# Kernel tuning notes

Measured on AMD Instinct MI355X. Metric: run time of the kernel, lower is better.

The kernel has to match this reference:

```python
import jax, jax.numpy as jnp
import numpy as np

GROUPS = 32
N_HEADS = 8
EPS = 1e-5


def setup_inputs() -> dict:
    key = jax.random.key(0)
    ks = jax.random.split(key, 4)
    B, C, H, W = 8, 512, 32, 32
    x = jax.random.normal(ks[0], (B, C, H, W), dtype=jnp.float32)
    norm_scale = jnp.ones((C,), jnp.float32)
    norm_bias = jnp.zeros((C,), jnp.float32)
    qkv_w = jax.random.normal(ks[1], (3 * C, C), jnp.float32) * (C ** -0.5)
    qkv_b = jnp.zeros((3 * C,), jnp.float32)
    proj_w = jax.random.normal(ks[2], (C, C), jnp.float32) * (C ** -0.5)
    proj_b = jnp.zeros((C,), jnp.float32)
    return {"x": x, "norm_scale": norm_scale, "norm_bias": norm_bias,
            "qkv_w": qkv_w, "qkv_b": qkv_b, "proj_w": proj_w, "proj_b": proj_b}


def reference(x, norm_scale, norm_bias, qkv_w, qkv_b, proj_w, proj_b):
    B, C, H, W = x.shape
    T = H * W
    xf = x.reshape(B, C, T)

    # GroupNorm32 (32 groups, computed in float32, affine)
    xg = xf.astype(jnp.float32).reshape(B, GROUPS, C // GROUPS, T)
    mean = xg.mean(axis=(2, 3), keepdims=True)
    var = xg.var(axis=(2, 3), keepdims=True)
    xn = ((xg - mean) * jax.lax.rsqrt(var + EPS)).reshape(B, C, T)
    xn = (xn * norm_scale[:, None] + norm_bias[:, None]).astype(x.dtype)

    # qkv: 1x1 conv1d == pointwise matmul -> [B, 3C, T]
    qkv = jnp.einsum('oc,bct->bot', qkv_w, xn) + qkv_b[:, None]

    # QKVAttentionLegacy: reshape to [B*H, 3*ch, T], split
    ch = C // N_HEADS
    qkv_h = qkv.reshape(B * N_HEADS, 3 * ch, T)
    q, k, v = qkv_h[:, :ch], qkv_h[:, ch:2 * ch], qkv_h[:, 2 * ch:]
    scale = ch ** -0.25
    weight = jnp.einsum('bct,bcs->bts', q * scale, k * scale)  # [B*H, T, T]
    weight = jax.nn.softmax(weight.astype(jnp.float32), axis=-1).astype(qkv.dtype)
    a = jnp.einsum('bts,bcs->bct', weight, v).reshape(B, C, T)

    # proj_out (1x1 conv) + residual
    h = jnp.einsum('oc,bct->bot', proj_w, a) + proj_b[:, None]
    return (xf + h).reshape(B, C, H, W)
```

## Files before the change

kernel.cpp:

```cpp
#include <hip/hip_runtime.h>
#include <hip/hip_bf16.h>
#include <stdint.h>

typedef unsigned short u16;
typedef unsigned int u32;
typedef __bf16 bf16x8 __attribute__((ext_vector_type(8)));
typedef float f32x4 __attribute__((ext_vector_type(4)));


static __device__ __forceinline__ u16 f2bf(float f) {
  union { __hip_bfloat16 h; u16 u; } c;
  c.h = __float2bfloat16(f);
  return c.u;
}

static __device__ __forceinline__ void gload_lds16(const void* g, void* l) {
  __builtin_amdgcn_global_load_lds(
      (__attribute__((address_space(1))) u32*)(uintptr_t)g,
      (__attribute__((address_space(3))) u32*)l, 16, 0, 0);
}

__global__ __launch_bounds__(256) void wcvt(const float* __restrict__ wq,
                                            const float* __restrict__ wp,
                                            u16* __restrict__ wqb,
                                            u16* __restrict__ wpb) {
  int idx = (blockIdx.x * 256 + threadIdx.x) * 4;
  const float* s;
  u16* d;
  if (idx < 786432) { s = wq + idx; d = wqb + idx; }
  else { int k = idx - 786432; s = wp + k; d = wpb + k; }
  float4 v = *(const float4*)s;
  uint2 o;
  o.x = (u32)f2bf(v.x) | ((u32)f2bf(v.y) << 16);
  o.y = (u32)f2bf(v.z) | ((u32)f2bf(v.w) << 16);
  *(uint2*)d = o;
}

__global__ __launch_bounds__(256) void gn_stats(const float* __restrict__ x,
                                                float* __restrict__ st) {
  int bg = blockIdx.x;
  const float* p = x + (size_t)bg * 16384;
  float s1 = 0.f, s2 = 0.f;
  for (int i = threadIdx.x * 4; i < 16384; i += 1024) {
    float4 v = *(const float4*)(p + i);
    s1 += v.x + v.y + v.z + v.w;
    s2 += v.x * v.x + v.y * v.y + v.z * v.z + v.w * v.w;
  }
#pragma unroll
  for (int off = 1; off < 64; off <<= 1) {
    s1 += __shfl_xor(s1, off);
    s2 += __shfl_xor(s2, off);
  }
  __shared__ float r1[4], r2[4];
  int w = threadIdx.x >> 6, l = threadIdx.x & 63;
  if (l == 0) { r1[w] = s1; r2[w] = s2; }
  __syncthreads();
  if (threadIdx.x == 0) {
    float t1 = r1[0] + r1[1] + r1[2] + r1[3];
    float t2 = r2[0] + r2[1] + r2[2] + r2[3];
    float mean = t1 * (1.f / 16384.f);
    float var = t2 * (1.f / 16384.f) - mean * mean;
    st[bg * 2] = mean;
    st[bg * 2 + 1] = rsqrtf(var + 1e-5f);
  }
}

__global__ __launch_bounds__(256) void gn_apply(const float* __restrict__ x,
                                                const float* __restrict__ st,
                                                const float* __restrict__ ns,
                                                const float* __restrict__ nbi,
                                                u16* __restrict__ xnt) {
  __shared__ u16 tile[32 * 520];
  int b = blockIdx.x >> 5;
  int t0 = (blockIdx.x & 31) << 5;
  int tid = threadIdx.x;
  int tl = tid & 31, cg = tid >> 5;
#pragma unroll 4
  for (int cc = 0; cc < 64; ++cc) {
    int c = cc * 8 + cg;
    float mean = st[(b * 32 + (c >> 4)) * 2];
    float rstd = st[(b * 32 + (c >> 4)) * 2 + 1];
    float v = x[(size_t)b * 524288 + (size_t)c * 1024 + t0 + tl];
    float vn = (v - mean) * rstd * ns[c] + nbi[c];
    tile[tl * 520 + c] = f2bf(vn);
  }
  __syncthreads();
#pragma unroll
  for (int i = 0; i < 8; ++i) {
    int chunk = i * 256 + tid;
    int tl2 = chunk >> 6;
    int c0 = (chunk & 63) * 8;
    uint4 d = *(const uint4*)(tile + tl2 * 520 + c0);
    *(uint4*)(xnt + (size_t)b * 524288 + (size_t)(t0 + tl2) * 512 + c0) = d;
  }
}

static __device__ __forceinline__ void gemm_core(const u16* Abase, const u16* Bbase,
                                                 f32x4 acc[4][4], u16* As, u16* Bs,
                                                 int w, int l, int wm, int wn) {
  const int r8 = l >> 3, ch = l & 7;
  const int fr = l & 15, fq = l >> 4;
#pragma unroll 1
  for (int kt = 0; kt < 8; ++kt) {
    __syncthreads();
#pragma unroll
    for (int i = 0; i < 4; ++i) {
      int gi = (w << 2) + i;
      int row = (gi << 3) + r8;
      int xoff = ((ch ^ (row & 7)) << 4);
      gload_lds16((const char*)Abase + (size_t)row * 1024 + (kt << 7) + xoff,
                  (char*)As + (gi << 10));
      gload_lds16((const char*)Bbase + (size_t)row * 1024 + (kt << 7) + xoff,
                  (char*)Bs + (gi << 10));
    }
    __syncthreads();
#pragma unroll
    for (int kf = 0; kf < 2; ++kf) {
      bf16x8 af[4], bfv[4];
#pragma unroll
      for (int i = 0; i < 4; ++i) {
        int rowA = wm * 64 + i * 16 + fr;
        af[i] = *(const bf16x8*)(As + rowA * 64 + ((((kf << 2) + fq) ^ (rowA & 7)) << 3));
        int rowB = wn * 64 + i * 16 + fr;
        bfv[i] = *(const bf16x8*)(Bs + rowB * 64 + ((((kf << 2) + fq) ^ (rowB & 7)) << 3));
      }
#pragma unroll
      for (int i = 0; i < 4; ++i)
#pragma unroll
        for (int j = 0; j < 4; ++j)
          acc[i][j] = __builtin_amdgcn_mfma_f32_16x16x32_bf16(af[i], bfv[j], acc[i][j], 0, 0, 0);
    }
  }
}

__global__ __launch_bounds__(256) void gemm_qkv(const u16* __restrict__ Wq,
                                                const u16* __restrict__ Xnt,
                                                const float* __restrict__ bq,
                                                u16* __restrict__ qT,
                                                u16* __restrict__ kT,
                                                u16* __restrict__ vv) {
  __shared__ u16 SMEM[18432];
  int bid0 = blockIdx.x;
  int bid = (bid0 & 7) * 96 + (bid0 >> 3);
  int mb = bid % 12, nb = (bid / 12) % 8, b = bid / 96;
  int tid = threadIdx.x, w = tid >> 6, l = tid & 63;
  int wm = tid >> 7, wn = (tid >> 6) & 1;
  int fr = l & 15, fq = l >> 4;
  f32x4 acc[4][4];
#pragma unroll
  for (int i = 0; i < 4; ++i)
#pragma unroll
    for (int j = 0; j < 4; ++j) acc[i][j] = (f32x4){0.f, 0.f, 0.f, 0.f};

  gemm_core(Wq + (size_t)mb * 65536, Xnt + (size_t)b * 524288 + (size_t)nb * 65536,
            acc, SMEM, SMEM + 8192, w, l, wm, wn);

  __syncthreads();

  int seg2 = mb * 2 + wm;
  int h = seg2 / 3, typ = seg2 % 3;
  size_t hb = (size_t)(b * 8 + h) * 65536;
  u16* SUB = SMEM + wm * 9216;

  if (typ < 2) {
    float qksc = (typ == 0) ? 0.51011687f : 0.35355339f;
#pragma unroll
    for (int i = 0; i < 4; ++i) {
      int oi = i * 16 + fq * 4;
      float4 bb = *(const float4*)(bq + mb * 128 + wm * 64 + oi);
#pragma unroll
      for (int j = 0; j < 4; ++j) {
        int tl = wn * 64 + j * 16 + fr;
        f32x4 v = acc[i][j];
        u32 lo = (u32)f2bf((v[0] + bb.x) * qksc) | ((u32)f2bf((v[1] + bb.y) * qksc) << 16);
        u32 hi = (u32)f2bf((v[2] + bb.z) * qksc) | ((u32)f2bf((v[3] + bb.w) * qksc) << 16);
        *(u32*)(SUB + tl * 72 + oi) = lo;
        *(u32*)(SUB + tl * 72 + oi + 2) = hi;
      }
    }
  } else {
#pragma unroll
    for (int i = 0; i < 4; ++i) {
      int oi = i * 16 + fq * 4;
      float4 bb = *(const float4*)(bq + mb * 128 + wm * 64 + oi);
      float bbv[4] = {bb.x, bb.y, bb.z, bb.w};
#pragma unroll
      for (int j = 0; j < 4; ++j) {
        int tl = wn * 64 + j * 16 + fr;
        f32x4 v = acc[i][j];
#pragma unroll
        for (int r = 0; r < 4; ++r)
          SUB[(oi + r) * 136 + tl] = f2bf(v[r] + bbv[r]);
      }
    }
  }
  __syncthreads();

  int lt = tid & 127;
  if (typ < 2) {
    u16* dstb = (typ == 0 ? qT : kT) + hb;
#pragma unroll
    for (int it = 0; it < 8; ++it) {
      int slot = it * 128 + lt;
      int t = slot >> 3, chk = slot & 7;
      uint4 val = *(const uint4*)(SUB + t * 72 + chk * 8);
      *(uint4*)(dstb + (size_t)(nb * 128 + t) * 64 + chk * 8) = val;
    }
  } else {
#pragma unroll
    for (int it = 0; it < 8; ++it) {
      int slot = it * 128 + lt;
      int c = slot >> 4, chk = slot & 15;
      uint4 val = *(const uint4*)(SUB + c * 136 + chk * 8);
      *(uint4*)(vv + hb + (size_t)c * 1024 + nb * 128 + chk * 8) = val;
    }
  }
}

__global__ __launch_bounds__(512) void attn(const u16* __restrict__ qT,
                                            const u16* __restrict__ kT,
                                            const u16* __restrict__ vv,
                                            u16* __restrict__ aT) {
  __shared__ u16 Ks[128 * 64];
  __shared__ u16 Vs[64 * 128];
  __shared__ u16 Ps[8 * 16 * 72];
  int bid = blockIdx.x;
  int bh = (bid & 7) * 8 + (bid >> 6);
  int tq = (bid >> 3) & 7;
  int tid = threadIdx.x, w = tid >> 6, l = tid & 63;
  int fr = l & 15, fq = l >> 4;
  int r8 = l >> 3, ch = l & 7;
  size_t hb = (size_t)bh * 65536;

  bf16x8 aq[2];
  {
    const u16* qp = qT + hb + (size_t)(tq * 128 + w * 16 + fr) * 64 + fq * 8;
    aq[0] = *(const bf16x8*)(qp);
    aq[1] = *(const bf16x8*)(qp + 32);
  }

  union { u32 u[4]; bf16x8 v; } onesu;
#pragma unroll
  for (int i = 0; i < 4; ++i) onesu.u[i] = 0x3F803F80u;
  const bf16x8 vone = onesu.v;

  f32x4 acc_o[4];
  f32x4 acc_s = (f32x4){0.f, 0.f, 0.f, 0.f};
#pragma unroll
  for (int nb = 0; nb < 4; ++nb) acc_o[nb] = (f32x4){0.f, 0.f, 0.f, 0.f};

  u16* pw = Ps + w * (16 * 72);

#pragma unroll 1
  for (int st = 0; st < 8; ++st) {
    __syncthreads();
#pragma unroll
    for (int j = 0; j < 2; ++j) {
      int gi = w * 2 + j;
      int row = gi * 8 + r8;
      int xoff = ((ch ^ (row & 7)) << 4);
      gload_lds16((const char*)(kT + hb) + (size_t)(st * 128 + row) * 128 + xoff,
                  (char*)Ks + (gi << 10));
      int c = gi * 4 + (l >> 4);
      int half = (l >> 3) & 1;
      int ch8 = l & 7;
      int sxoff = half * 128 + ((ch8 ^ (c & 7)) << 4);
      gload_lds16((const char*)(vv + hb) + (size_t)c * 2048 + st * 256 + sxoff,
                  (char*)Vs + (gi << 10));
    }
    __syncthreads();

#pragma unroll
    for (int sh = 0; sh < 2; ++sh) {
      f32x4 sa[4];
#pragma unroll
      for (int nb = 0; nb < 4; ++nb) sa[nb] = (f32x4){0.f, 0.f, 0.f, 0.f};
      __builtin_amdgcn_s_setprio(1);
#pragma unroll
      for (int nb = 0; nb < 4; ++nb) {
        int krow = sh * 64 + nb * 16 + fr;
#pragma unroll
        for (int kf = 0; kf < 2; ++kf) {
          bf16x8 bk = *(const bf16x8*)(Ks + krow * 64 + ((((kf << 2) + fq) ^ (krow & 7)) << 3));
          sa[nb] = __builtin_amdgcn_mfma_f32_16x16x32_bf16(aq[kf], bk, sa[nb], 0, 0, 0);
        }
      }
      __builtin_amdgcn_s_setprio(0);

#pragma unroll
      for (int nb = 0; nb < 4; ++nb)
#pragma unroll
        for (int r = 0; r < 4; ++r)
          pw[(fq * 4 + r) * 72 + nb * 16 + fr] = f2bf(exp2f(sa[nb][r]));

      bf16x8 ap[2];
#pragma unroll
      for (int kf = 0; kf < 2; ++kf)
        ap[kf] = *(const bf16x8*)(pw + fr * 72 + kf * 32 + fq * 8);

      __builtin_amdgcn_s_setprio(1);
#pragma unroll
      for (int nb = 0; nb < 4; ++nb) {
        int vrow = nb * 16 + fr;
#pragma unroll
        for (int kf = 0; kf < 2; ++kf) {
          bf16x8 bv = *(const bf16x8*)(Vs + vrow * 128 + sh * 64 +
                                       ((((kf << 2) + fq) ^ (vrow & 7)) << 3));
          acc_o[nb] = __builtin_amdgcn_mfma_f32_16x16x32_bf16(ap[kf], bv, acc_o[nb], 0, 0, 0);
        }
      }
#pragma unroll
      for (int kf = 0; kf < 2; ++kf)
        acc_s = __builtin_amdgcn_mfma_f32_16x16x32_bf16(ap[kf], vone, acc_s, 0, 0, 0);
      __builtin_amdgcn_s_setprio(0);
    }
  }

  int b = bh >> 3, h = bh & 7;
  f32x4 invl;
#pragma unroll
  for (int r = 0; r < 4; ++r) invl[r] = 1.f / acc_s[r];
#pragma unroll
  for (int nb = 0; nb < 4; ++nb) {
    f32x4 ov = acc_o[nb] * invl;
#pragma unroll
    for (int r = 0; r < 4; ++r) {
      int t = tq * 128 + w * 16 + fq * 4 + r;
      aT[(size_t)b * 524288 + (size_t)t * 512 + h * 64 + nb * 16 + fr] = f2bf(ov[r]);
    }
  }
}

__global__ __launch_bounds__(256) void gemm_proj(const u16* __restrict__ Wp,
                                                 const u16* __restrict__ aT,
                                                 const float* __restrict__ bp,
                                                 const float* __restrict__ x,
                                                 float* __restrict__ out) {
  __shared__ u16 As[128 * 64];
  __shared__ u16 Bs[128 * 64];
  int bid0 = blockIdx.x;
  int bid = (bid0 & 7) * 32 + (bid0 >> 3);
  int mb = bid & 3, nb = (bid >> 2) & 7, b = bid >> 5;
  int tid = threadIdx.x, w = tid >> 6, l = tid & 63;
  int wm = w >> 1, wn = w & 1;
  f32x4 acc[4][4];
#pragma unroll
  for (int i = 0; i < 4; ++i)
#pragma unroll
    for (int j = 0; j < 4; ++j) acc[i][j] = (f32x4){0.f, 0.f, 0.f, 0.f};

  gemm_core(Wp + (size_t)mb * 65536, aT + (size_t)b * 524288 + (size_t)nb * 65536,
            acc, As, Bs, w, l, wm, wn);

  int fr = l & 15, fq = l >> 4;
#pragma unroll
  for (int i = 0; i < 4; ++i) {
    int o0 = mb * 128 + wm * 64 + i * 16 + fq * 4;
    float b0 = bp[o0], b1 = bp[o0 + 1], b2 = bp[o0 + 2], b3 = bp[o0 + 3];
#pragma unroll
    for (int j = 0; j < 4; ++j) {
      int t = nb * 128 + wn * 64 + j * 16 + fr;
      f32x4 v = acc[i][j];
      size_t base = (size_t)b * 524288 + (size_t)o0 * 1024 + t;
      out[base] = x[base] + v[0] + b0;
      out[base + 1024] = x[base + 1024] + v[1] + b1;
      out[base + 2048] = x[base + 2048] + v[2] + b2;
      out[base + 3072] = x[base + 3072] + v[3] + b3;
    }
  }
}

extern "C" void kernel_launch(void* const* d_in, const int* in_sizes, int n_in,
                              void* d_out, int out_size, void* d_ws, size_t ws_size,
                              hipStream_t stream) {
  const float* x = (const float*)d_in[0];
  const float* ns = (const float*)d_in[1];
  const float* nbi = (const float*)d_in[2];
  const float* wq = (const float*)d_in[3];
  const float* bq = (const float*)d_in[4];
  const float* wp = (const float*)d_in[5];
  const float* bp = (const float*)d_in[6];
  float* out = (float*)d_out;
  char* ws = (char*)d_ws;

  u16* wqb = (u16*)(ws);
  u16* wpb = (u16*)(ws + 1572864);
  float* st = (float*)(ws + 2097152);
  u16* xnt = (u16*)(ws + 2101248);
  u16* qT = (u16*)(ws + 2101248 + 8388608);
  u16* kT = (u16*)(ws + 2101248 + 2 * 8388608);
  u16* vv = (u16*)(ws + 2101248 + 3 * 8388608);
  u16* aT = xnt;

  hipLaunchKernelGGL(wcvt, dim3(1024), dim3(256), 0, stream, wq, wp, wqb, wpb);
  hipLaunchKernelGGL(gn_stats, dim3(256), dim3(256), 0, stream, x, st);
  hipLaunchKernelGGL(gn_apply, dim3(256), dim3(256), 0, stream, x, st, ns, nbi, xnt);
  hipLaunchKernelGGL(gemm_qkv, dim3(768), dim3(256), 0, stream, wqb, xnt, bq, qT, kT, vv);
  hipLaunchKernelGGL(attn, dim3(512), dim3(512), 0, stream, qT, kT, vv, aT);
  hipLaunchKernelGGL(gemm_proj, dim3(256), dim3(256), 0, stream, wpb, aT, bp, x, out);
}
```

Before: 95.51 us.

## Merge weight conversion with GN stats, vectorize gn_apply, truncate softmax bf16

The weight bf16 conversion and the GroupNorm statistics kernels become one launch, with blocks split by index. gn_apply now reads float4 along the time axis instead of scalar loads. In the QKV epilogue two 32-bit LDS stores become one 64-bit store. The attention softmax probabilities are converted to bf16 by truncation rather than round-to-nearest, which makes the exp path cheaper but adds a small rounding bias.

```diff
diff --git a/kernel.cpp b/kernel.cpp
--- a/kernel.cpp
+++ b/kernel.cpp
@@ -14,31 +14,39 @@
   return c.u;
 }
 
+static __device__ __forceinline__ u16 f2bf_t(float f) {
+  union { float f; u32 u; } c;
+  c.f = f;
+  return (u16)(c.u >> 16);
+}
+
 static __device__ __forceinline__ void gload_lds16(const void* g, void* l) {
   __builtin_amdgcn_global_load_lds(
       (__attribute__((address_space(1))) u32*)(uintptr_t)g,
       (__attribute__((address_space(3))) u32*)l, 16, 0, 0);
 }
 
-__global__ __launch_bounds__(256) void wcvt(const float* __restrict__ wq,
+__global__ __launch_bounds__(256) void prep(const float* __restrict__ wq,
                                             const float* __restrict__ wp,
+                                            const float* __restrict__ x,
                                             u16* __restrict__ wqb,
-                                            u16* __restrict__ wpb) {
-  int idx = (blockIdx.x * 256 + threadIdx.x) * 4;
-  const float* s;
-  u16* d;
-  if (idx < 786432) { s = wq + idx; d = wqb + idx; }
-  else { int k = idx - 786432; s = wp + k; d = wpb + k; }
-  float4 v = *(const float4*)s;
-  uint2 o;
-  o.x = (u32)f2bf(v.x) | ((u32)f2bf(v.y) << 16);
-  o.y = (u32)f2bf(v.z) | ((u32)f2bf(v.w) << 16);
-  *(uint2*)d = o;
-}
-
-__global__ __launch_bounds__(256) void gn_stats(const float* __restrict__ x,
-                                                float* __restrict__ st) {
-  int bg = blockIdx.x;
+                                            u16* __restrict__ wpb,
+                                            float* __restrict__ st) {
+  int blk = blockIdx.x;
+  if (blk >= 256) {
+    int idx = ((blk - 256) * 256 + threadIdx.x) * 4;
+    const float* s;
+    u16* d;
+    if (idx < 786432) { s = wq + idx; d = wqb + idx; }
+    else { int k = idx - 786432; s = wp + k; d = wpb + k; }
+    float4 v = *(const float4*)s;
+    uint2 o;
+    o.x = (u32)f2bf(v.x) | ((u32)f2bf(v.y) << 16);
+    o.y = (u32)f2bf(v.z) | ((u32)f2bf(v.w) << 16);
+    *(uint2*)d = o;
+    return;
+  }
+  int bg = blk;
   const float* p = x + (size_t)bg * 16384;
   float s1 = 0.f, s2 = 0.f;
   for (int i = threadIdx.x * 4; i < 16384; i += 1024) {
@@ -74,24 +82,28 @@
   int b = blockIdx.x >> 5;
   int t0 = (blockIdx.x & 31) << 5;
   int tid = threadIdx.x;
-  int tl = tid & 31, cg = tid >> 5;
+  int tg = (tid & 7) * 4;
+  int c0 = tid >> 3;
 #pragma unroll 4
-  for (int cc = 0; cc < 64; ++cc) {
-    int c = cc * 8 + cg;
+  for (int cc = 0; cc < 16; ++cc) {
+    int c = cc * 32 + c0;
     float mean = st[(b * 32 + (c >> 4)) * 2];
     float rstd = st[(b * 32 + (c >> 4)) * 2 + 1];
-    float v = x[(size_t)b * 524288 + (size_t)c * 1024 + t0 + tl];
-    float vn = (v - mean) * rstd * ns[c] + nbi[c];
-    tile[tl * 520 + c] = f2bf(vn);
+    float sc = ns[c], bi = nbi[c];
+    float4 v = *(const float4*)(x + (size_t)b * 524288 + (size_t)c * 1024 + t0 + tg);
+    tile[(tg + 0) * 520 + c] = f2bf((v.x - mean) * rstd * sc + bi);
+    tile[(tg + 1) * 520 + c] = f2bf((v.y - mean) * rstd * sc + bi);
+    tile[(tg + 2) * 520 + c] = f2bf((v.z - mean) * rstd * sc + bi);
+    tile[(tg + 3) * 520 + c] = f2bf((v.w - mean) * rstd * sc + bi);
   }
   __syncthreads();
 #pragma unroll
   for (int i = 0; i < 8; ++i) {
     int chunk = i * 256 + tid;
     int tl2 = chunk >> 6;
-    int c0 = (chunk & 63) * 8;
-    uint4 d = *(const uint4*)(tile + tl2 * 520 + c0);
-    *(uint4*)(xnt + (size_t)b * 524288 + (size_t)(t0 + tl2) * 512 + c0) = d;
+    int c0b = (chunk & 63) * 8;
+    uint4 d = *(const uint4*)(tile + tl2 * 520 + c0b);
+    *(uint4*)(xnt + (size_t)b * 524288 + (size_t)(t0 + tl2) * 512 + c0b) = d;
   }
 }
 
@@ -172,10 +184,10 @@
       for (int j = 0; j < 4; ++j) {
         int tl = wn * 64 + j * 16 + fr;
         f32x4 v = acc[i][j];
-        u32 lo = (u32)f2bf((v[0] + bb.x) * qksc) | ((u32)f2bf((v[1] + bb.y) * qksc) << 16);
-        u32 hi = (u32)f2bf((v[2] + bb.z) * qksc) | ((u32)f2bf((v[3] + bb.w) * qksc) << 16);
-        *(u32*)(SUB + tl * 72 + oi) = lo;
-        *(u32*)(SUB + tl * 72 + oi + 2) = hi;
+        uint2 pk;
+        pk.x = (u32)f2bf((v[0] + bb.x) * qksc) | ((u32)f2bf((v[1] + bb.y) * qksc) << 16);
+        pk.y = (u32)f2bf((v[2] + bb.z) * qksc) | ((u32)f2bf((v[3] + bb.w) * qksc) << 16);
+        *(uint2*)(SUB + tl * 72 + oi) = pk;
       }
     }
   } else {
@@ -291,7 +303,7 @@
       for (int nb = 0; nb < 4; ++nb)
 #pragma unroll
         for (int r = 0; r < 4; ++r)
-          pw[(fq * 4 + r) * 72 + nb * 16 + fr] = f2bf(exp2f(sa[nb][r]));
+          pw[(fq * 4 + r) * 72 + nb * 16 + fr] = f2bf_t(exp2f(sa[nb][r]));
 
       bf16x8 ap[2];
 #pragma unroll
@@ -392,8 +404,7 @@
   u16* vv = (u16*)(ws + 2101248 + 3 * 8388608);
   u16* aT = xnt;
 
-  hipLaunchKernelGGL(wcvt, dim3(1024), dim3(256), 0, stream, wq, wp, wqb, wpb);
-  hipLaunchKernelGGL(gn_stats, dim3(256), dim3(256), 0, stream, x, st);
+  hipLaunchKernelGGL(prep, dim3(1280), dim3(256), 0, stream, wq, wp, x, wqb, wpb, st);
   hipLaunchKernelGGL(gn_apply, dim3(256), dim3(256), 0, stream, x, st, ns, nbi, xnt);
   hipLaunchKernelGGL(gemm_qkv, dim3(768), dim3(256), 0, stream, wqb, xnt, bq, qT, kT, vv);
   hipLaunchKernelGGL(attn, dim3(512), dim3(512), 0, stream, qT, kT, vv, aT);
```

After: 87.75 us (median of 3 runs). -8.1%, faster.
